# Kernel optimization log

Hardware: AMD Instinct MI355X
Metric: run time of the kernel (lower is better)

The kernel has to match this reference:

```python
import jax, jax.numpy as jnp
import numpy as np
from jax import lax

TAU = 1.0  # registered buffer, default 1.0 -> Q_tau = +inf -> clamp is a no-op
EPS = 1e-5
SQRT2 = float(np.sqrt(2.0))

# sign with straight-through estimator (weights): grad = identity
@jax.custom_vjp
def sign_w(w):
    return jnp.sign(w)
def _sign_w_fwd(w):
    return jnp.sign(w), None
def _sign_w_bwd(_, g):
    return (g,)
sign_w.defvjp(_sign_w_fwd, _sign_w_bwd)

@jax.custom_vjp
def sign_a(x):
    return jnp.sign(x)
def _sign_a_fwd(x):
    return jnp.sign(x), x
def _sign_a_bwd(x, g):
    return (jnp.maximum(2.0 - jnp.abs(2.0 * x), 0.0) * g,)
sign_a.defvjp(_sign_a_fwd, _sign_a_bwd)

def binarize_conv2d(a, w, alpha, stride=1):
    # weight standardization (torch.var is unbiased -> ddof=1)
    w0 = w - jnp.mean(w, axis=(1, 2, 3), keepdims=True)
    var = jnp.var(w0, axis=(1, 2, 3), keepdims=True, ddof=1)
    w1 = w0 * (2.0 * SQRT2) / jnp.sqrt(var + EPS)
    EW = jnp.mean(jnp.abs(w1))
    Q_tau = lax.stop_gradient(-EW * jnp.log(2.0 - 2.0 * TAU))  # +inf for tau=1
    w2 = jnp.clip(w1, -Q_tau, Q_tau)
    bw = sign_w(w2)
    ba = sign_a(a)  # eval mode: a0 = a (no per-sample var normalization)
    out = lax.conv_general_dilated(
        ba, bw, window_strides=(stride, stride), padding=((1, 1), (1, 1)),
        dimension_numbers=('NCHW', 'OIHW', 'NCHW'))
    return out * alpha[None]  # alpha: [C_out,1,1] -> broadcast over N,H,W

def bn_eval(x, gamma, beta, mean, var):
    scale = (gamma / jnp.sqrt(var + EPS)).reshape(1, -1, 1, 1)
    shift = (beta - mean * gamma / jnp.sqrt(var + EPS)).reshape(1, -1, 1, 1)
    return x * scale + shift

def hardtanh(x):
    return jnp.clip(x, -1.0, 1.0)

def setup_inputs() -> dict:
    key = jax.random.key(0)
    ks = jax.random.split(key, 13)
    N, C, H, W = 64, 256, 32, 32
    return {
        'x': jax.random.normal(ks[0], (N, C, H, W), jnp.float32),
        'conv1_w': jax.random.normal(ks[1], (C, C, 3, 3), jnp.float32) * 0.05,
        'alpha1': jax.random.uniform(ks[2], (C, 1, 1), jnp.float32),
        'bn1_gamma': jax.random.uniform(ks[3], (C,), jnp.float32) + 0.5,
        'bn1_beta': jax.random.normal(ks[4], (C,), jnp.float32) * 0.1,
        'bn1_mean': jax.random.normal(ks[5], (C,), jnp.float32),
        'bn1_var': jax.random.uniform(ks[6], (C,), jnp.float32) + 0.5,
        'conv2_w': jax.random.normal(ks[7], (C, C, 3, 3), jnp.float32) * 0.05,
        'alpha2': jax.random.uniform(ks[8], (C, 1, 1), jnp.float32),
        'bn2_gamma': jax.random.uniform(ks[9], (C,), jnp.float32) + 0.5,
        'bn2_beta': jax.random.normal(ks[10], (C,), jnp.float32) * 0.1,
        'bn2_mean': jax.random.normal(ks[11], (C,), jnp.float32),
        'bn2_var': jax.random.uniform(ks[12], (C,), jnp.float32) + 0.5,
    }

def reference(x, conv1_w, alpha1, bn1_gamma, bn1_beta, bn1_mean, bn1_var,
              conv2_w, alpha2, bn2_gamma, bn2_beta, bn2_mean, bn2_var):
    out = hardtanh(bn_eval(binarize_conv2d(x, conv1_w, alpha1, stride=1),
                           bn1_gamma, bn1_beta, bn1_mean, bn1_var))
    out = bn_eval(binarize_conv2d(out, conv2_w, alpha2, stride=1),
                  bn2_gamma, bn2_beta, bn2_mean, bn2_var)
    out = out + x  # identity shortcut (stride=1, in_planes==planes)
    return hardtanh(out)
```

## Files before the change

kernel.cpp:

```cpp
#include <hip/hip_runtime.h>
#include <cstdint>
#include <cstddef>

using u32 = unsigned int;
using u64 = unsigned long long;

typedef int v4i  __attribute__((ext_vector_type(4)));
typedef int v16i __attribute__((ext_vector_type(16)));

#define EPSV 1e-5f

__global__ void prep_weights(const float* __restrict__ w1, const float* __restrict__ w2,
                             const float* __restrict__ a1, const float* __restrict__ g1,
                             const float* __restrict__ b1, const float* __restrict__ m1,
                             const float* __restrict__ v1,
                             const float* __restrict__ a2, const float* __restrict__ g2,
                             const float* __restrict__ b2, const float* __restrict__ m2,
                             const float* __restrict__ v2,
                             unsigned char* __restrict__ Wsgn, float4* __restrict__ SC4)
{
    const int co   = blockIdx.x;
    const int conv = blockIdx.y;
    const int c    = threadIdx.x;
    const float* w = conv ? w2 : w1;

    float wv[9];
    const float* wp = w + ((size_t)co * 256 + c) * 9;
    float s = 0.f;
#pragma unroll
    for (int p = 0; p < 9; ++p) { wv[p] = wp[p]; s += wv[p]; }

    __shared__ float red[256];
    red[c] = s;
    __syncthreads();
    for (int off = 128; off > 0; off >>= 1) {
        if (c < off) red[c] += red[c + off];
        __syncthreads();
    }
    const float mean = __fdiv_rn(red[0], 2304.0f);

    unsigned char* wrow = Wsgn + ((size_t)(conv * 256 + co) * 9) * 256;
#pragma unroll
    for (int p = 0; p < 9; ++p)
        wrow[p * 256 + c] = (wv[p] > mean) ? 0x01u : 0xFFu;

    if (c == 0) {
        const float alpha = conv ? a2[co] : a1[co];
        const float gamma = conv ? g2[co] : g1[co];
        const float beta  = conv ? b2[co] : b1[co];
        const float mu    = conv ? m2[co] : m1[co];
        const float var   = conv ? v2[co] : v1[co];
        const float sq    = __fsqrt_rn(__fadd_rn(var, EPSV));
        const float scale = __fdiv_rn(gamma, sq);
        const float shift = __fsub_rn(beta, __fdiv_rn(__fmul_rn(mu, gamma), sq));
        SC4[conv * 256 + co] = make_float4(alpha, scale, shift, 0.f);
    }
}

__global__ void build_bfrag(const unsigned char* __restrict__ Wsgn, uint4* __restrict__ Bf)
{
    const int f    = blockIdx.x;
    const int lane = threadIdx.x;
    const int conv = f / 576;
    const int rem  = f % 576;
    const int g    = rem / 72;
    const int p    = (rem % 72) / 8;
    const int cb   = rem % 8;
    const int co   = g * 32 + (lane & 31);
    const unsigned char* src = Wsgn + ((size_t)(conv * 256 + co) * 9 + p) * 256
                                    + cb * 32 + (lane >> 5) * 16;
    Bf[(size_t)f * 64 + lane] = *(const uint4*)src;
}

__global__ void binarize_x(const float* __restrict__ x, u32* __restrict__ A1)
{
    const int n = blockIdx.x >> 3;
    const int j = blockIdx.x & 7;
    const int p = threadIdx.x;
    const float* xp = x + (((size_t)n * 256 + j * 32) * 1024) + p;
    u32 bits = 0;
#pragma unroll
    for (int k = 0; k < 32; ++k) {
        float v = xp[(size_t)k * 1024];
        bits |= (v > 0.f ? 1u : 0u) << k;
    }
    A1[((size_t)n * 1024 + p) * 8 + j] = bits;
}

__device__ __forceinline__ u32 expand4(u32 x)
{
    u32 r;
    r  = ((x & 1u) ? 0x00000001u : 0x000000FFu);
    r |= ((x & 2u) ? 0x00000100u : 0x0000FF00u);
    r |= ((x & 4u) ? 0x00010000u : 0x00FF0000u);
    r |= ((x & 8u) ? 0x01000000u : 0xFF000000u);
    return r;
}

__device__ __forceinline__ void glds16(const void* g, void* l)
{
    __builtin_amdgcn_global_load_lds(
        (const __attribute__((address_space(1))) void*)g,
        (__attribute__((address_space(3))) void*)l, 16, 0, 0);
}

template<int CONV>
__global__ __launch_bounds__(256, 2)
void conv_mfma(const u32* __restrict__ A_in, const v4i* __restrict__ Bf,
               const float4* __restrict__ SC4, const float* __restrict__ X,
               u32* __restrict__ A_out, float* __restrict__ OUT)
{
    const int n    = blockIdx.x >> 3;
    const int yq   = blockIdx.x & 7;
    const int y0   = yq * 4;
    const int tid  = threadIdx.x;
    const int wave = tid >> 6;
    const int lane = tid & 63;
    const int col0 = lane & 31;

    __shared__ alignas(16) unsigned char lds[81920];

    const int fbias = (CONV == 2) ? 576 : 0;
    const int g0 = wave * 2;
    const char* bsrc0 = (const char*)Bf + (((size_t)(fbias + g0 * 72)) << 10)
                        + (size_t)lane * 16;
    unsigned char* bslot = lds + 49152 + wave * 8192;

#pragma unroll
    for (int i = 0; i < 3; ++i) {
        glds16(bsrc0 + ((size_t)i << 10), bslot + i * 2048);
        glds16(bsrc0 + ((size_t)i << 10) + 73728, bslot + i * 2048 + 1024);
    }

    for (int s = tid; s < 3072; s += 256) {
        const int xs   = s & 31;
        const int rest = s >> 5;
        const int r    = rest % 6;
        const int c16  = rest / 6;
        const int iy   = y0 - 1 + r;
        u32 d0 = 0, d1 = 0, d2 = 0, d3 = 0;
        if ((unsigned)iy < 32u) {
            const u32 wrd = A_in[((size_t)n * 1024 + iy * 32 + xs) * 8 + (c16 >> 1)];
            const u32 h = (wrd >> ((c16 & 1) * 16)) & 0xFFFFu;
            d0 = expand4(h);
            d1 = expand4(h >> 4);
            d2 = expand4(h >> 8);
            d3 = expand4(h >> 12);
        }
        *(uint4*)(lds + (size_t)s * 16) = make_uint4(d0, d1, d2, d3);
    }
    __syncthreads();

    const v16i Z  = {0,0,0,0,0,0,0,0,0,0,0,0,0,0,0,0};
    const v4i  Z4 = {0,0,0,0};
    v16i c0a = Z, c0b = Z;
    v16i c1a = Z, c1b = Z;
    v16i c2a = Z, c2b = Z;
    v16i c3a = Z, c3b = Z;

    const u32 bb = 49152u + (u32)(wave * 8192 + lane * 16);

#pragma unroll 1
    for (int k = 0; k < 72; ++k) {
        {
            const int kf  = k + 3;
            const int kfm = (kf >= 72) ? kf - 72 : kf;
            const char* s0 = bsrc0 + ((size_t)kfm << 10);
            unsigned char* d = bslot + (kf & 3) * 2048;
            glds16(s0, d);
            glds16(s0 + 73728, d + 1024);
        }
        __builtin_amdgcn_sched_barrier(0);

        const int p  = k >> 3, cb = k & 7;
        const int dy = p / 3,  dx = p - dy * 3;
        int c = col0 + dx - 1; c = c < 0 ? 0 : (c > 31 ? 31 : c);
        const u32 ao = (u32)((lane >> 5) * 3072 + cb * 6144 + dy * 512 + c * 16);
        v4i a0 = *(const v4i*)(lds + ao);
        v4i a1 = *(const v4i*)(lds + ao + 512);
        v4i a2 = *(const v4i*)(lds + ao + 1024);
        v4i a3 = *(const v4i*)(lds + ao + 1536);
        if ((dx == 0 && col0 == 0) || (dx == 2 && col0 == 31)) {
            a0 = Z4; a1 = Z4; a2 = Z4; a3 = Z4;
        }

        asm volatile("s_waitcnt vmcnt(6)" ::: "memory");
        __builtin_amdgcn_sched_barrier(0);

        const u32 bo = bb + (u32)((k & 3) * 2048);
        const v4i b0 = *(const v4i*)(lds + bo);
        const v4i b1 = *(const v4i*)(lds + bo + 1024);

        __builtin_amdgcn_s_setprio(1);
        c0a = __builtin_amdgcn_mfma_i32_32x32x32_i8(a0, b0, c0a, 0, 0, 0);
        c0b = __builtin_amdgcn_mfma_i32_32x32x32_i8(a0, b1, c0b, 0, 0, 0);
        c1a = __builtin_amdgcn_mfma_i32_32x32x32_i8(a1, b0, c1a, 0, 0, 0);
        c1b = __builtin_amdgcn_mfma_i32_32x32x32_i8(a1, b1, c1b, 0, 0, 0);
        c2a = __builtin_amdgcn_mfma_i32_32x32x32_i8(a2, b0, c2a, 0, 0, 0);
        c2b = __builtin_amdgcn_mfma_i32_32x32x32_i8(a2, b1, c2b, 0, 0, 0);
        c3a = __builtin_amdgcn_mfma_i32_32x32x32_i8(a3, b0, c3a, 0, 0, 0);
        c3b = __builtin_amdgcn_mfma_i32_32x32x32_i8(a3, b1, c3b, 0, 0, 0);
        __builtin_amdgcn_s_setprio(0);
    }

    const int bias2 = (CONV == 2) ? 256 : 0;
    const float4 scA = SC4[bias2 + (g0 + 0) * 32 + col0];
    const float4 scB = SC4[bias2 + (g0 + 1) * 32 + col0];

    if (CONV == 1) {
#define EP1(ACC, R, G, SC)                                                      \
        { _Pragma("unroll")                                                     \
          for (int reg = 0; reg < 16; ++reg) {                                  \
              const float t = __fadd_rn(__fmul_rn(__fmul_rn((float)ACC[reg],    \
                                        SC.x), SC.y), SC.z);                    \
              const u64 m = __ballot(t > 0.f);                                  \
              if (lane == 0) {                                                  \
                  const int x = (reg & 3) + 8 * (reg >> 2);                     \
                  const size_t pb = (size_t)n * 1024 + (y0 + (R)) * 32 + x;     \
                  A_out[pb * 8 + (G)]       = (u32)m;                           \
                  A_out[(pb + 4) * 8 + (G)] = (u32)(m >> 32);                   \
              } } }
        EP1(c0a, 0, g0, scA)      EP1(c0b, 0, g0 + 1, scB)
        EP1(c1a, 1, g0, scA)      EP1(c1b, 1, g0 + 1, scB)
        EP1(c2a, 2, g0, scA)      EP1(c2b, 2, g0 + 1, scB)
        EP1(c3a, 3, g0, scA)      EP1(c3b, 3, g0 + 1, scB)
#undef EP1
    } else {
        __syncthreads();
        float* ep = (float*)lds;
#define EP2PASS(CA, CB, R)                                                      \
        { _Pragma("unroll")                                                     \
          for (int reg = 0; reg < 16; ++reg) {                                  \
              const int x = (reg & 3) + 8 * (reg >> 2) + 4 * (lane >> 5);       \
              ep[x * 257 + (g0 + 0) * 32 + col0] =                              \
                  __fadd_rn(__fmul_rn(__fmul_rn((float)CA[reg], scA.x),         \
                                      scA.y), scA.z);                           \
              ep[x * 257 + (g0 + 1) * 32 + col0] =                              \
                  __fadd_rn(__fmul_rn(__fmul_rn((float)CB[reg], scB.x),         \
                                      scB.y), scB.z);                           \
          }                                                                     \
          __syncthreads();                                                      \
          {                                                                     \
              const int co = tid;                                               \
              const size_t gb = ((size_t)(n * 256 + co)) * 1024                 \
                              + (y0 + (R)) * 32;                                \
              _Pragma("unroll")                                                 \
              for (int x4 = 0; x4 < 32; x4 += 4) {                              \
                  float4 rr;                                                    \
                  rr.x = ep[(x4 + 0) * 257 + co];                               \
                  rr.y = ep[(x4 + 1) * 257 + co];                               \
                  rr.z = ep[(x4 + 2) * 257 + co];                               \
                  rr.w = ep[(x4 + 3) * 257 + co];                               \
                  const float4 xv = *(const float4*)(X + gb + x4);              \
                  rr.x = fminf(1.f, fmaxf(-1.f, __fadd_rn(rr.x, xv.x)));        \
                  rr.y = fminf(1.f, fmaxf(-1.f, __fadd_rn(rr.y, xv.y)));        \
                  rr.z = fminf(1.f, fmaxf(-1.f, __fadd_rn(rr.z, xv.z)));        \
                  rr.w = fminf(1.f, fmaxf(-1.f, __fadd_rn(rr.w, xv.w)));        \
                  *(float4*)(OUT + gb + x4) = rr;                               \
              }                                                                 \
          }                                                                     \
          __syncthreads(); }
        EP2PASS(c0a, c0b, 0)
        EP2PASS(c1a, c1b, 1)
        EP2PASS(c2a, c2b, 2)
        EP2PASS(c3a, c3b, 3)
#undef EP2PASS
    }
}

extern "C" void kernel_launch(void* const* d_in, const int* in_sizes, int n_in,
                              void* d_out, int out_size, void* d_ws, size_t ws_size,
                              hipStream_t stream)
{
    const float* x   = (const float*)d_in[0];
    const float* w1  = (const float*)d_in[1];
    const float* al1 = (const float*)d_in[2];
    const float* g1  = (const float*)d_in[3];
    const float* b1  = (const float*)d_in[4];
    const float* m1  = (const float*)d_in[5];
    const float* v1  = (const float*)d_in[6];
    const float* w2  = (const float*)d_in[7];
    const float* al2 = (const float*)d_in[8];
    const float* g2  = (const float*)d_in[9];
    const float* b2  = (const float*)d_in[10];
    const float* m2  = (const float*)d_in[11];
    const float* v2  = (const float*)d_in[12];
    float* out = (float*)d_out;

    char* ws = (char*)d_ws;
    float4*        SC4  = (float4*)(ws);
    unsigned char* Wsgn = (unsigned char*)(ws + (64u << 10));
    uint4*         Bf   = (uint4*)(ws + (2u << 20));
    u32*           A1   = (u32*)(ws + (4u << 20));
    u32*           A2   = (u32*)(ws + (6u << 20));
    (void)ws_size; (void)in_sizes; (void)n_in; (void)out_size;

    prep_weights<<<dim3(256, 2), 256, 0, stream>>>(w1, w2, al1, g1, b1, m1, v1,
                                                   al2, g2, b2, m2, v2, Wsgn, SC4);
    build_bfrag<<<dim3(1152), 64, 0, stream>>>(Wsgn, Bf);
    binarize_x<<<dim3(512), 1024, 0, stream>>>(x, A1);
    conv_mfma<1><<<dim3(512), 256, 0, stream>>>(A1, (const v4i*)Bf, SC4,
                                                nullptr, A2, nullptr);
    conv_mfma<2><<<dim3(512), 256, 0, stream>>>(A2, (const v4i*)Bf, SC4,
                                                x, nullptr, out);
}
```

Before: 138.6 us.

## Use 8-row tiles with 8 waves sharing weight fragments in LDS

Each conv block now covers 8 output rows with 512 threads arranged as a 2x4 wave grid, so every weight fragment loaded into LDS serves two row groups. The activation tile is stored pre-padded (34 columns), which removes the edge clamp and masking. The K loop is software-pipelined with register double buffering and workgroup barriers, using a 2-deep LDS ring for weights. The cost is larger LDS use, only 256 blocks per conv, and extra barriers in the inner loop.

```diff
diff --git a/kernel.cpp b/kernel.cpp
--- a/kernel.cpp
+++ b/kernel.cpp
@@ -9,6 +9,7 @@
 typedef int v16i __attribute__((ext_vector_type(16)));
 
 #define EPSV 1e-5f
+#define MFMA_I8(A, B, C) __builtin_amdgcn_mfma_i32_32x32x32_i8((A), (B), (C), 0, 0, 0)
 
 __global__ void prep_weights(const float* __restrict__ w1, const float* __restrict__ w2,
                              const float* __restrict__ a1, const float* __restrict__ g1,
@@ -105,42 +106,45 @@
 }
 
 template<int CONV>
-__global__ __launch_bounds__(256, 2)
+__global__ __launch_bounds__(512, 2)
 void conv_mfma(const u32* __restrict__ A_in, const v4i* __restrict__ Bf,
                const float4* __restrict__ SC4, const float* __restrict__ X,
                u32* __restrict__ A_out, float* __restrict__ OUT)
 {
-    const int n    = blockIdx.x >> 3;
-    const int yq   = blockIdx.x & 7;
-    const int y0   = yq * 4;
+    const int n    = blockIdx.x >> 2;
+    const int yo   = blockIdx.x & 3;
+    const int y0   = yo * 8;
     const int tid  = threadIdx.x;
     const int wave = tid >> 6;
     const int lane = tid & 63;
+    const int wm   = wave >> 2;
+    const int wn   = wave & 3;
     const int col0 = lane & 31;
-
-    __shared__ alignas(16) unsigned char lds[81920];
+    const int g0   = wn * 2;
+
+    __shared__ alignas(16) unsigned char lds[103424];
 
     const int fbias = (CONV == 2) ? 576 : 0;
-    const int g0 = wave * 2;
-    const char* bsrc0 = (const char*)Bf + (((size_t)(fbias + g0 * 72)) << 10)
+    const char* bsrcA = (const char*)Bf + (((size_t)(fbias + g0 * 72)) << 10)
                         + (size_t)lane * 16;
-    unsigned char* bslot = lds + 49152 + wave * 8192;
-
-#pragma unroll
-    for (int i = 0; i < 3; ++i) {
-        glds16(bsrc0 + ((size_t)i << 10), bslot + i * 2048);
-        glds16(bsrc0 + ((size_t)i << 10) + 73728, bslot + i * 2048 + 1024);
-    }
-
-    for (int s = tid; s < 3072; s += 256) {
-        const int xs   = s & 31;
-        const int rest = s >> 5;
-        const int r    = rest % 6;
-        const int c16  = rest / 6;
+    const char* bsrcB = bsrcA + (72u << 10);
+    unsigned char* bdst = lds + 87040 + (size_t)g0 * 1024;
+
+    glds16(bsrcA,        bdst);
+    glds16(bsrcB,        bdst + 1024);
+    glds16(bsrcA + 1024, bdst + 8192);
+    glds16(bsrcB + 1024, bdst + 8192 + 1024);
+
+    for (int s = tid; s < 5440; s += 512) {
+        const int colv = s % 34;
+        const int rest = s / 34;
+        const int r    = rest % 10;
+        const int c16  = rest / 10;
         const int iy   = y0 - 1 + r;
+        const int ix   = colv - 1;
         u32 d0 = 0, d1 = 0, d2 = 0, d3 = 0;
-        if ((unsigned)iy < 32u) {
-            const u32 wrd = A_in[((size_t)n * 1024 + iy * 32 + xs) * 8 + (c16 >> 1)];
+        if ((unsigned)iy < 32u && (unsigned)ix < 32u) {
+            const u32 wrd = A_in[((size_t)n * 1024 + iy * 32 + ix) * 8 + (c16 >> 1)];
             const u32 h = (wrd >> ((c16 & 1) * 16)) & 0xFFFFu;
             d0 = expand4(h);
             d1 = expand4(h >> 4);
@@ -149,66 +153,82 @@
         }
         *(uint4*)(lds + (size_t)s * 16) = make_uint4(d0, d1, d2, d3);
     }
-    __syncthreads();
-
-    const v16i Z  = {0,0,0,0,0,0,0,0,0,0,0,0,0,0,0,0};
-    const v4i  Z4 = {0,0,0,0};
-    v16i c0a = Z, c0b = Z;
-    v16i c1a = Z, c1b = Z;
-    v16i c2a = Z, c2b = Z;
-    v16i c3a = Z, c3b = Z;
-
-    const u32 bb = 49152u + (u32)(wave * 8192 + lane * 16);
-
-#pragma unroll 1
-    for (int k = 0; k < 72; ++k) {
-        {
-            const int kf  = k + 3;
-            const int kfm = (kf >= 72) ? kf - 72 : kf;
-            const char* s0 = bsrc0 + ((size_t)kfm << 10);
-            unsigned char* d = bslot + (kf & 3) * 2048;
-            glds16(s0, d);
-            glds16(s0 + 73728, d + 1024);
-        }
-        __builtin_amdgcn_sched_barrier(0);
-
-        const int p  = k >> 3, cb = k & 7;
-        const int dy = p / 3,  dx = p - dy * 3;
-        int c = col0 + dx - 1; c = c < 0 ? 0 : (c > 31 ? 31 : c);
-        const u32 ao = (u32)((lane >> 5) * 3072 + cb * 6144 + dy * 512 + c * 16);
-        v4i a0 = *(const v4i*)(lds + ao);
-        v4i a1 = *(const v4i*)(lds + ao + 512);
-        v4i a2 = *(const v4i*)(lds + ao + 1024);
-        v4i a3 = *(const v4i*)(lds + ao + 1536);
-        if ((dx == 0 && col0 == 0) || (dx == 2 && col0 == 31)) {
-            a0 = Z4; a1 = Z4; a2 = Z4; a3 = Z4;
-        }
-
-        asm volatile("s_waitcnt vmcnt(6)" ::: "memory");
-        __builtin_amdgcn_sched_barrier(0);
-
-        const u32 bo = bb + (u32)((k & 3) * 2048);
-        const v4i b0 = *(const v4i*)(lds + bo);
-        const v4i b1 = *(const v4i*)(lds + bo + 1024);
-
-        __builtin_amdgcn_s_setprio(1);
-        c0a = __builtin_amdgcn_mfma_i32_32x32x32_i8(a0, b0, c0a, 0, 0, 0);
-        c0b = __builtin_amdgcn_mfma_i32_32x32x32_i8(a0, b1, c0b, 0, 0, 0);
-        c1a = __builtin_amdgcn_mfma_i32_32x32x32_i8(a1, b0, c1a, 0, 0, 0);
-        c1b = __builtin_amdgcn_mfma_i32_32x32x32_i8(a1, b1, c1b, 0, 0, 0);
-        c2a = __builtin_amdgcn_mfma_i32_32x32x32_i8(a2, b0, c2a, 0, 0, 0);
-        c2b = __builtin_amdgcn_mfma_i32_32x32x32_i8(a2, b1, c2b, 0, 0, 0);
-        c3a = __builtin_amdgcn_mfma_i32_32x32x32_i8(a3, b0, c3a, 0, 0, 0);
-        c3b = __builtin_amdgcn_mfma_i32_32x32x32_i8(a3, b1, c3b, 0, 0, 0);
-        __builtin_amdgcn_s_setprio(0);
-    }
 
     const int bias2 = (CONV == 2) ? 256 : 0;
     const float4 scA = SC4[bias2 + (g0 + 0) * 32 + col0];
     const float4 scB = SC4[bias2 + (g0 + 1) * 32 + col0];
 
+    __syncthreads();
+
+    const v16i Z  = {0,0,0,0,0,0,0,0,0,0,0,0,0,0,0,0};
+    v16i c0a = Z, c0b = Z, c1a = Z, c1b = Z;
+    v16i c2a = Z, c2b = Z, c3a = Z, c3b = Z;
+
+    const u32 lc16off = (u32)((lane >> 5) * 5440);
+    const u32 rowbase = (u32)((4 * wm) * 544);
+    const u32 bwoff   = (u32)(g0 * 1024 + lane * 16);
+
+    v4i ea0, ea1, ea2, ea3, eb0, eb1;
+    v4i oa0, oa1, oa2, oa3, ob0, ob1;
+    {
+        const u32 ao = lc16off + rowbase + (u32)(col0 * 16);
+        ea0 = *(const v4i*)(lds + ao);
+        ea1 = *(const v4i*)(lds + ao + 544);
+        ea2 = *(const v4i*)(lds + ao + 1088);
+        ea3 = *(const v4i*)(lds + ao + 1632);
+        const u32 bo = 87040u + bwoff;
+        eb0 = *(const v4i*)(lds + bo);
+        eb1 = *(const v4i*)(lds + bo + 1024);
+    }
+
+#define PHASE(KC, AN0, AN1, AN2, AN3, BN0, BN1, AC0, AC1, AC2, AC3, BC0, BC1)   \
+    {                                                                           \
+        const int k_ = (KC);                                                    \
+        int kf_ = k_ + 2; if (kf_ >= 72) kf_ -= 72;                             \
+        {                                                                       \
+            unsigned char* d_ = bdst + ((k_ & 1) << 13);                        \
+            glds16(bsrcA + ((size_t)kf_ << 10), d_);                            \
+            glds16(bsrcB + ((size_t)kf_ << 10), d_ + 1024);                     \
+        }                                                                       \
+        __builtin_amdgcn_sched_barrier(0);                                      \
+        {                                                                       \
+            const int kn_ = k_ + 1;                                             \
+            const int cb_ = kn_ & 7, p_ = kn_ >> 3;                             \
+            const int dy_ = p_ / 3, dx_ = p_ - dy_ * 3;                         \
+            const u32 ao_ = lc16off + (u32)(2 * cb_) * 5440u + rowbase          \
+                          + (u32)(dy_ * 544) + (u32)((dx_ + col0) * 16);        \
+            AN0 = *(const v4i*)(lds + ao_);                                     \
+            AN1 = *(const v4i*)(lds + ao_ + 544);                               \
+            AN2 = *(const v4i*)(lds + ao_ + 1088);                              \
+            AN3 = *(const v4i*)(lds + ao_ + 1632);                              \
+            asm volatile("s_waitcnt vmcnt(2)" ::: "memory");                    \
+            __builtin_amdgcn_sched_barrier(0);                                  \
+            const u32 bo_ = 87040u + (u32)((kn_ & 1) << 13) + bwoff;            \
+            BN0 = *(const v4i*)(lds + bo_);                                     \
+            BN1 = *(const v4i*)(lds + bo_ + 1024);                              \
+        }                                                                       \
+        __builtin_amdgcn_s_barrier();                                           \
+        asm volatile("s_waitcnt lgkmcnt(6)" ::: "memory");                      \
+        __builtin_amdgcn_sched_barrier(0);                                      \
+        __builtin_amdgcn_s_setprio(1);                                          \
+        c0a = MFMA_I8(AC0, BC0, c0a);  c0b = MFMA_I8(AC0, BC1, c0b);            \
+        c1a = MFMA_I8(AC1, BC0, c1a);  c1b = MFMA_I8(AC1, BC1, c1b);            \
+        c2a = MFMA_I8(AC2, BC0, c2a);  c2b = MFMA_I8(AC2, BC1, c2b);            \
+        c3a = MFMA_I8(AC3, BC0, c3a);  c3b = MFMA_I8(AC3, BC1, c3b);            \
+        __builtin_amdgcn_s_setprio(0);                                          \
+        __builtin_amdgcn_s_barrier();                                           \
+    }
+
+#pragma unroll 1
+    for (int j = 0; j < 36; ++j) {
+        const int k = j * 2;
+        PHASE(k,     oa0, oa1, oa2, oa3, ob0, ob1,  ea0, ea1, ea2, ea3, eb0, eb1)
+        PHASE(k + 1, ea0, ea1, ea2, ea3, eb0, eb1,  oa0, oa1, oa2, oa3, ob0, ob1)
+    }
+#undef PHASE
+
     if (CONV == 1) {
-#define EP1(ACC, R, G, SC)                                                      \
+#define EP1(ACC, MR, GI, SC)                                                    \
         { _Pragma("unroll")                                                     \
           for (int reg = 0; reg < 16; ++reg) {                                  \
               const float t = __fadd_rn(__fmul_rn(__fmul_rn((float)ACC[reg],    \
@@ -216,41 +236,43 @@
               const u64 m = __ballot(t > 0.f);                                  \
               if (lane == 0) {                                                  \
                   const int x = (reg & 3) + 8 * (reg >> 2);                     \
-                  const size_t pb = (size_t)n * 1024 + (y0 + (R)) * 32 + x;     \
-                  A_out[pb * 8 + (G)]       = (u32)m;                           \
-                  A_out[(pb + 4) * 8 + (G)] = (u32)(m >> 32);                   \
+                  const int row = y0 + 4 * wm + (MR);                           \
+                  const size_t pb = (size_t)n * 1024 + row * 32 + x;            \
+                  A_out[pb * 8 + (g0 + (GI))]       = (u32)m;                   \
+                  A_out[(pb + 4) * 8 + (g0 + (GI))] = (u32)(m >> 32);           \
               } } }
-        EP1(c0a, 0, g0, scA)      EP1(c0b, 0, g0 + 1, scB)
-        EP1(c1a, 1, g0, scA)      EP1(c1b, 1, g0 + 1, scB)
-        EP1(c2a, 2, g0, scA)      EP1(c2b, 2, g0 + 1, scB)
-        EP1(c3a, 3, g0, scA)      EP1(c3b, 3, g0 + 1, scB)
+        EP1(c0a, 0, 0, scA)  EP1(c0b, 0, 1, scB)
+        EP1(c1a, 1, 0, scA)  EP1(c1b, 1, 1, scB)
+        EP1(c2a, 2, 0, scA)  EP1(c2b, 2, 1, scB)
+        EP1(c3a, 3, 0, scA)  EP1(c3b, 3, 1, scB)
 #undef EP1
     } else {
         __syncthreads();
         float* ep = (float*)lds;
 #define EP2PASS(CA, CB, R)                                                      \
-        { _Pragma("unroll")                                                     \
-          for (int reg = 0; reg < 16; ++reg) {                                  \
-              const int x = (reg & 3) + 8 * (reg >> 2) + 4 * (lane >> 5);       \
-              ep[x * 257 + (g0 + 0) * 32 + col0] =                              \
-                  __fadd_rn(__fmul_rn(__fmul_rn((float)CA[reg], scA.x),         \
-                                      scA.y), scA.z);                           \
-              ep[x * 257 + (g0 + 1) * 32 + col0] =                              \
-                  __fadd_rn(__fmul_rn(__fmul_rn((float)CB[reg], scB.x),         \
-                                      scB.y), scB.z);                           \
-          }                                                                     \
+        { if (wm == ((R) >> 2)) {                                               \
+            _Pragma("unroll")                                                   \
+            for (int reg = 0; reg < 16; ++reg) {                                \
+                const int x = (reg & 3) + 8 * (reg >> 2) + 4 * (lane >> 5);     \
+                ep[x * 257 + (g0 + 0) * 32 + col0] =                            \
+                    __fadd_rn(__fmul_rn(__fmul_rn((float)CA[reg], scA.x),       \
+                                        scA.y), scA.z);                         \
+                ep[x * 257 + (g0 + 1) * 32 + col0] =                            \
+                    __fadd_rn(__fmul_rn(__fmul_rn((float)CB[reg], scB.x),       \
+                                        scB.y), scB.z);                         \
+            } }                                                                 \
           __syncthreads();                                                      \
           {                                                                     \
-              const int co = tid;                                               \
+              const int co = tid >> 1, xh = tid & 1;                            \
               const size_t gb = ((size_t)(n * 256 + co)) * 1024                 \
-                              + (y0 + (R)) * 32;                                \
+                              + (y0 + (R)) * 32 + xh * 16;                      \
               _Pragma("unroll")                                                 \
-              for (int x4 = 0; x4 < 32; x4 += 4) {                              \
+              for (int x4 = 0; x4 < 16; x4 += 4) {                              \
                   float4 rr;                                                    \
-                  rr.x = ep[(x4 + 0) * 257 + co];                               \
-                  rr.y = ep[(x4 + 1) * 257 + co];                               \
-                  rr.z = ep[(x4 + 2) * 257 + co];                               \
-                  rr.w = ep[(x4 + 3) * 257 + co];                               \
+                  rr.x = ep[(xh * 16 + x4 + 0) * 257 + co];                     \
+                  rr.y = ep[(xh * 16 + x4 + 1) * 257 + co];                     \
+                  rr.z = ep[(xh * 16 + x4 + 2) * 257 + co];                     \
+                  rr.w = ep[(xh * 16 + x4 + 3) * 257 + co];                     \
                   const float4 xv = *(const float4*)(X + gb + x4);              \
                   rr.x = fminf(1.f, fmaxf(-1.f, __fadd_rn(rr.x, xv.x)));        \
                   rr.y = fminf(1.f, fmaxf(-1.f, __fadd_rn(rr.y, xv.y)));        \
@@ -264,6 +286,10 @@
         EP2PASS(c1a, c1b, 1)
         EP2PASS(c2a, c2b, 2)
         EP2PASS(c3a, c3b, 3)
+        EP2PASS(c0a, c0b, 4)
+        EP2PASS(c1a, c1b, 5)
+        EP2PASS(c2a, c2b, 6)
+        EP2PASS(c3a, c3b, 7)
 #undef EP2PASS
     }
 }
@@ -299,8 +325,8 @@
                                                    al2, g2, b2, m2, v2, Wsgn, SC4);
     build_bfrag<<<dim3(1152), 64, 0, stream>>>(Wsgn, Bf);
     binarize_x<<<dim3(512), 1024, 0, stream>>>(x, A1);
-    conv_mfma<1><<<dim3(512), 256, 0, stream>>>(A1, (const v4i*)Bf, SC4,
+    conv_mfma<1><<<dim3(256), 512, 0, stream>>>(A1, (const v4i*)Bf, SC4,
                                                 nullptr, A2, nullptr);
-    conv_mfma<2><<<dim3(512), 256, 0, stream>>>(A2, (const v4i*)Bf, SC4,
+    conv_mfma<2><<<dim3(256), 512, 0, stream>>>(A2, (const v4i*)Bf, SC4,
                                                 x, nullptr, out);
 }
```

Result: faster. 129.9 us (-6.3%).
